# Optimization experiments

Measured on AMD Instinct MI355X. Metric: run time of the kernel, lower is better.

Reference implementation:

```python
import jax, jax.numpy as jnp
import numpy as np

N, E, F_IN, DIM, G = 50000, 800000, 128, 128, 512
NUM_GC_LAYERS = 3
S2S_STEPS = 3


def setup_inputs() -> dict:
    key = jax.random.key(0)
    ks = jax.random.split(key, 17)
    s = 0.05
    rn = lambda k, shape: jax.random.normal(k, shape, jnp.float32) * s
    x = jax.random.normal(ks[0], (N, F_IN), jnp.float32)
    edge_index = jax.random.randint(ks[1], (2, E), 0, N)
    batch = jnp.sort(jax.random.randint(ks[2], (N,), 0, G))
    return dict(
        x=x, edge_index=edge_index, batch=batch,
        lin0_W=rn(ks[3], (DIM, F_IN)), lin0_b=rn(ks[4], (DIM,)),
        gin_W1=rn(ks[5], (DIM, DIM)), gin_b1=rn(ks[6], (DIM,)),
        gin_W2=rn(ks[7], (DIM, DIM)), gin_b2=rn(ks[8], (DIM,)),
        gru_Wih=rn(ks[9], (3 * DIM, DIM)), gru_Whh=rn(ks[10], (3 * DIM, DIM)),
        gru_bih=rn(ks[11], (3 * DIM,)), gru_bhh=rn(ks[12], (3 * DIM,)),
        lstm_Wih=rn(ks[13], (4 * DIM, 2 * DIM)), lstm_Whh=rn(ks[14], (4 * DIM, DIM)),
        lstm_bih=rn(ks[15], (4 * DIM,)), lstm_bhh=rn(ks[16], (4 * DIM,)),
    )


def reference(x, edge_index, batch, lin0_W, lin0_b, gin_W1, gin_b1, gin_W2, gin_b2,
              gru_Wih, gru_Whh, gru_bih, gru_bhh,
              lstm_Wih, lstm_Whh, lstm_bih, lstm_bhh):
    src, dst = edge_index[0], edge_index[1]
    out = jax.nn.relu(x @ lin0_W.T + lin0_b)          # [N, DIM]
    h = out                                            # GRU hidden (seq_len=1, 1 layer)
    for _ in range(NUM_GC_LAYERS):
        # GINConv, eps=0: nn(x + sum_{j in N(i)} x_j); scatter-add over edge list
        aggr = jax.ops.segment_sum(out[src], dst, num_segments=N)
        z = out + aggr
        m = jax.nn.relu(jax.nn.relu(z @ gin_W1.T + gin_b1) @ gin_W2.T + gin_b2)
        # single GRU step (PyTorch gate order: r, z, n)
        gx = m @ gru_Wih.T + gru_bih
        gh = h @ gru_Whh.T + gru_bhh
        gxr, gxz, gxn = jnp.split(gx, 3, axis=-1)
        ghr, ghz, ghn = jnp.split(gh, 3, axis=-1)
        r = jax.nn.sigmoid(gxr + ghr)
        zt = jax.nn.sigmoid(gxz + ghz)
        n = jnp.tanh(gxn + r * ghn)
        h = (1.0 - zt) * n + zt * h
        out = h
    # Set2Set pooling (processing_steps=3), LSTM(2*DIM -> DIM), gate order i,f,g,o
    q_star = jnp.zeros((G, 2 * DIM), x.dtype)
    hl = jnp.zeros((G, DIM), x.dtype)
    cl = jnp.zeros((G, DIM), x.dtype)
    for _ in range(S2S_STEPS):
        gates = q_star @ lstm_Wih.T + lstm_bih + hl @ lstm_Whh.T + lstm_bhh
        i, f, g, o = jnp.split(gates, 4, axis=-1)
        cl = jax.nn.sigmoid(f) * cl + jax.nn.sigmoid(i) * jnp.tanh(g)
        hl = jax.nn.sigmoid(o) * jnp.tanh(cl)
        q = hl                                          # [G, DIM]
        e = jnp.sum(out * q[batch], axis=-1)            # [N] attention logits
        emax = jax.lax.stop_gradient(jax.ops.segment_max(e, batch, num_segments=G))
        emax = jnp.where(jnp.isfinite(emax), emax, 0.0)
        a_num = jnp.exp(e - emax[batch])
        denom = jax.ops.segment_sum(a_num, batch, num_segments=G)
        a = a_num / (denom[batch] + 1e-16)              # per-graph softmax
        rvec = jax.ops.segment_sum(a[:, None] * out, batch, num_segments=G)
        q_star = jnp.concatenate([q, rvec], axis=-1)    # [G, 2*DIM]
    return (q_star, out)
```

## Files before the change

### kernel.cpp

```cpp
#include <hip/hip_runtime.h>
#include <hip/hip_bf16.h>
#include <math.h>

static constexpr int NN  = 50000;
static constexpr int NE  = 800000;
static constexpr int DIM = 128;
static constexpr int NG  = 512;
static constexpr int NBLK = (NN + 255) / 256;

typedef __attribute__((ext_vector_type(8))) short bf16x8;
typedef __attribute__((ext_vector_type(4))) float f32x4;
typedef __attribute__((ext_vector_type(8))) float f32x8;

__device__ __forceinline__ float sigm(float x) {
    return __builtin_amdgcn_rcpf(1.0f + __expf(-x));
}
__device__ __forceinline__ float ftanh(float x) {
    x = fminf(fmaxf(x, -15.f), 15.f);
    float t = __expf(2.f * x);
    return (t - 1.f) * __builtin_amdgcn_rcpf(t + 1.f);
}
__device__ __forceinline__ float b2f(ushort u) { return __uint_as_float(((unsigned)u) << 16); }
__device__ __forceinline__ ushort f2b(float f) {
    __hip_bfloat16 h = __float2bfloat16(f);
    return *reinterpret_cast<ushort*>(&h);
}
__device__ __forceinline__ bf16x8 ldb8(const ushort* p) {
    return *reinterpret_cast<const bf16x8*>(p);
}
__device__ __forceinline__ f32x8 acc8(f32x8 a, uint4 v) {
    a[0] += b2f(v.x & 0xffff); a[1] += b2f(v.x >> 16);
    a[2] += b2f(v.y & 0xffff); a[3] += b2f(v.y >> 16);
    a[4] += b2f(v.z & 0xffff); a[5] += b2f(v.z >> 16);
    a[6] += b2f(v.w & 0xffff); a[7] += b2f(v.w >> 16);
    return a;
}

__global__ __launch_bounds__(256) void k_prep(const float* __restrict__ lin0_W,
                                              const float* __restrict__ gin_W1,
                                              const float* __restrict__ gin_W2,
                                              const float* __restrict__ gru_Wih,
                                              const float* __restrict__ gru_Whh,
                                              const float* __restrict__ gru_bih,
                                              const float* __restrict__ gru_bhh,
                                              const float* __restrict__ lstm_Wih,
                                              const float* __restrict__ lstm_Whh,
                                              const float* __restrict__ lstm_bih,
                                              const float* __restrict__ lstm_bhh,
                                              const int* __restrict__ batch,
                                              ushort* __restrict__ wlin0,
                                              ushort* __restrict__ wg1,
                                              ushort* __restrict__ wg2,
                                              ushort* __restrict__ wihb,
                                              ushort* __restrict__ whhb,
                                              ushort* __restrict__ wrz,
                                              float* __restrict__ brz,
                                              unsigned* __restrict__ wp,
                                              float* __restrict__ bl,
                                              int* __restrict__ gstart,
                                              int* __restrict__ bcnt) {
    const int S0 = 16384, S1 = S0 + 16384, S2 = S1 + 16384;
    const int S3 = S2 + 49152, S4 = S3 + 49152, S5 = S4 + 65536;
    const int S6 = S5 + 256, S7 = S6 + 98304, S8 = S7 + 512;
    const int S9 = S8 + (NG + 1), S10 = S9 + 256;
    int i = blockIdx.x * 256 + threadIdx.x;
    if (i < S0) { wlin0[i] = f2b(lin0_W[i]); }
    else if (i < S1) { int j = i - S0; wg1[j] = f2b(gin_W1[j]); }
    else if (i < S2) { int j = i - S1; wg2[j] = f2b(gin_W2[j]); }
    else if (i < S3) { int j = i - S2; wihb[j] = f2b(gru_Wih[j]); }
    else if (i < S4) { int j = i - S3; whhb[j] = f2b(gru_Whh[j]); }
    else if (i < S5) {
        int j = i - S4; int col = j >> 8, k = j & 255;
        int row = (col >> 7) * 128 + (col & 127);
        wrz[j] = f2b((k < 128) ? gru_Whh[row * 128 + k] : gru_Wih[row * 128 + (k - 128)]);
    }
    else if (i < S6) { int j = i - S5; brz[j] = gru_bih[j] + gru_bhh[j]; }
    else if (i < S7) {
        int j = i - S6; int pk = j / 512, col = j % 512;
        int k0 = 2 * pk, k1 = 2 * pk + 1;
        float v0 = (k0 < 256) ? lstm_Wih[(size_t)col * 256 + k0]
                              : lstm_Whh[(size_t)col * 128 + (k0 - 256)];
        float v1 = (k1 < 256) ? lstm_Wih[(size_t)col * 256 + k1]
                              : lstm_Whh[(size_t)col * 128 + (k1 - 256)];
        wp[j] = ((unsigned)f2b(v1) << 16) | (unsigned)f2b(v0);
    }
    else if (i < S8) { int j = i - S7; bl[j] = lstm_bih[j] + lstm_bhh[j]; }
    else if (i < S9) {
        int g = i - S8;
        int lo = 0, hi = NN;
        while (lo < hi) { int mid = (lo + hi) >> 1; if (batch[mid] < g) lo = mid + 1; else hi = mid; }
        gstart[g] = lo;
    }
    else if (i < S10) { bcnt[i - S9] = 0; }
}
static constexpr int PREP_TOTAL = 16384 * 3 + 49152 * 2 + 65536 + 256 + 98304 + 512 + (NG + 1) + 256;

__global__ __launch_bounds__(256) void k_bcount(const int* __restrict__ dst,
                                                int* __restrict__ bcnt, int e) {
    __shared__ int l[256];
    int tid = threadIdx.x;
    l[tid] = 0;
    __syncthreads();
    int base = blockIdx.x * 4096;
    #pragma unroll
    for (int k = 0; k < 16; ++k) {
        int e0 = base + k * 256 + tid;
        if (e0 < e) atomicAdd(&l[dst[e0] >> 8], 1);
    }
    __syncthreads();
    if (l[tid] > 0) atomicAdd(&bcnt[tid], l[tid]);
}

__global__ __launch_bounds__(256) void k_btop(const int* __restrict__ bcnt,
                                              int* __restrict__ bbase,
                                              int* __restrict__ bcur) {
    __shared__ int s[256];
    int t = threadIdx.x;
    int v = bcnt[t];
    s[t] = v;
    __syncthreads();
    #pragma unroll
    for (int off = 1; off < 256; off <<= 1) {
        int x = (t >= off) ? s[t - off] : 0;
        __syncthreads();
        s[t] += x;
        __syncthreads();
    }
    int ex = s[t] - v;
    bbase[t] = ex;
    bcur[t] = ex;
    if (t == 255) bbase[256] = s[255];
}

__global__ __launch_bounds__(256) void k_bucket_lin0(const int* __restrict__ src,
                                                     const int* __restrict__ dst,
                                                     int* __restrict__ bcur,
                                                     int2* __restrict__ pairs, int e,
                                                     const float* __restrict__ X,
                                                     const ushort* __restrict__ W,
                                                     const float* __restrict__ bias,
                                                     ushort* __restrict__ AB, int n) {
    if (blockIdx.x < (unsigned)NBLK) {
        __shared__ int lcnt[256];
        __shared__ int lbase[256];
        int tid = threadIdx.x;
        lcnt[tid] = 0;
        __syncthreads();
        int base = blockIdx.x * 4096;
        #pragma unroll
        for (int k = 0; k < 16; ++k) {
            int e0 = base + k * 256 + tid;
            if (e0 < e) atomicAdd(&lcnt[dst[e0] >> 8], 1);
        }
        __syncthreads();
        int cnt = lcnt[tid];
        if (cnt > 0) lbase[tid] = atomicAdd(&bcur[tid], cnt);
        __syncthreads();
        lcnt[tid] = 0;
        __syncthreads();
        #pragma unroll
        for (int k = 0; k < 16; ++k) {
            int e0 = base + k * 256 + tid;
            if (e0 < e) {
                int d = dst[e0];
                int b = d >> 8;
                int off = atomicAdd(&lcnt[b], 1);
                pairs[lbase[b] + off] = make_int2(src[e0], d);
            }
        }
        return;
    }
    int bid = blockIdx.x - NBLK;
    int nlb = gridDim.x - NBLK;
    int lane = threadIdx.x & 63, wave = threadIdx.x >> 6;
    int c0 = lane & 15, kg = (lane >> 4) * 8;
    int tb0 = wave * 32;
    bf16x8 B[2][4];
    #pragma unroll
    for (int t = 0; t < 2; ++t)
        #pragma unroll
        for (int kk = 0; kk < 4; ++kk)
            B[t][kk] = ldb8(W + (size_t)(tb0 + t * 16 + c0) * 128 + kk * 32 + kg);

    for (int m0 = bid * 64; m0 < n; m0 += nlb * 64) {
        f32x4 acc[4][2];
        #pragma unroll
        for (int m = 0; m < 4; ++m) { acc[m][0] = {0,0,0,0}; acc[m][1] = {0,0,0,0}; }
        #pragma unroll
        for (int kk = 0; kk < 4; ++kk) {
            #pragma unroll
            for (int m = 0; m < 4; ++m) {
                int ar = min(m0 + m * 16 + c0, n - 1);
                const float* a = X + (size_t)ar * 128 + kk * 32 + kg;
                float4 x0 = *reinterpret_cast<const float4*>(a);
                float4 x1 = *reinterpret_cast<const float4*>(a + 4);
                bf16x8 af;
                af[0] = (short)f2b(x0.x); af[1] = (short)f2b(x0.y);
                af[2] = (short)f2b(x0.z); af[3] = (short)f2b(x0.w);
                af[4] = (short)f2b(x1.x); af[5] = (short)f2b(x1.y);
                af[6] = (short)f2b(x1.z); af[7] = (short)f2b(x1.w);
                acc[m][0] = __builtin_amdgcn_mfma_f32_16x16x32_bf16(af, B[0][kk], acc[m][0], 0, 0, 0);
                acc[m][1] = __builtin_amdgcn_mfma_f32_16x16x32_bf16(af, B[1][kk], acc[m][1], 0, 0, 0);
            }
        }
        #pragma unroll
        for (int m = 0; m < 4; ++m) {
            int rbase = m0 + m * 16 + ((lane >> 4) << 2);
            #pragma unroll
            for (int t = 0; t < 2; ++t) {
                int col = tb0 + t * 16 + c0;
                float bv = bias[col];
                #pragma unroll
                for (int j = 0; j < 4; ++j) {
                    int row = rbase + j;
                    if (row < n) {
                        float v = fmaxf(acc[m][t][j] + bv, 0.f);
                        AB[(size_t)row * 128 + col] = f2b(v);
                    }
                }
            }
        }
    }
}

__global__ __launch_bounds__(256) void k_fillbkt2(const int2* __restrict__ pairs,
                                                  const int* __restrict__ bbase,
                                                  int* __restrict__ rowptr,
                                                  int* __restrict__ csr) {
    __shared__ int lcnt[256];
    __shared__ int s[256];
    __shared__ int lcur[256];
    int b = blockIdx.x, tid = threadIdx.x;
    int w0 = b << 8;
    int r0 = bbase[b], r1 = bbase[b + 1];
    lcnt[tid] = 0;
    __syncthreads();
    for (int i = r0 + tid; i < r1; i += 256)
        atomicAdd(&lcnt[pairs[i].y - w0], 1);
    __syncthreads();
    int v = lcnt[tid];
    s[tid] = v;
    __syncthreads();
    #pragma unroll
    for (int off = 1; off < 256; off <<= 1) {
        int x = (tid >= off) ? s[tid - off] : 0;
        __syncthreads();
        s[tid] += x;
        __syncthreads();
    }
    int ex = r0 + s[tid] - v;
    lcur[tid] = ex;
    if (w0 + tid < NN) rowptr[w0 + tid] = ex;
    if (b == 0 && tid == 0) rowptr[NN] = NE;
    __syncthreads();
    for (int i = r0 + tid; i < r1; i += 256) {
        int2 p = pairs[i];
        int pos = atomicAdd(&lcur[p.y - w0], 1);
        csr[pos] = p.x;
    }
}

__global__ __launch_bounds__(512) void k_aggmlp(const ushort* __restrict__ AB,
                                                const int* __restrict__ rowptr,
                                                const int* __restrict__ csr,
                                                const ushort* __restrict__ W1,
                                                const float* __restrict__ b1,
                                                const ushort* __restrict__ W2,
                                                const float* __restrict__ b2,
                                                ushort* __restrict__ mt, int n) {
    __shared__ ushort Z_lds[32 * 136];
    __shared__ ushort M_lds[32 * 136];
    int tid = threadIdx.x;
    int lane = tid & 63, wave = tid >> 6;
    int c0 = lane & 15, kg = (lane >> 4) * 8;
    int colw = wave * 16 + c0;
    int rj = (lane >> 4) << 2;
    int grow_r = tid >> 4;
    int segi = tid & 15;
    const int stride = gridDim.x * 32;

    bf16x8 B1[4], B2[4];
    #pragma unroll
    for (int kk = 0; kk < 4; ++kk) {
        B1[kk] = ldb8(W1 + (size_t)colw * 128 + kk * 32 + kg);
        B2[kk] = ldb8(W2 + (size_t)colw * 128 + kk * 32 + kg);
    }
    float bv1 = b1[colw], bv2 = b2[colw];
    const uint4* bp = (const uint4*)AB;

    for (int m0 = blockIdx.x * 32; m0 < n; m0 += stride) {
        f32x8 A0 = {0,0,0,0,0,0,0,0};
        int grow = m0 + grow_r;
        if (grow < n) {
            f32x8 A1 = {0,0,0,0,0,0,0,0}, A2 = {0,0,0,0,0,0,0,0}, A3 = {0,0,0,0,0,0,0,0};
            A0 = acc8(A0, bp[(size_t)grow * 16 + segi]);
            int p = rowptr[grow], p1 = rowptr[grow + 1];
            for (; p + 4 <= p1; p += 4) {
                uint4 v0 = bp[(size_t)csr[p + 0] * 16 + segi];
                uint4 v1 = bp[(size_t)csr[p + 1] * 16 + segi];
                uint4 v2 = bp[(size_t)csr[p + 2] * 16 + segi];
                uint4 v3 = bp[(size_t)csr[p + 3] * 16 + segi];
                A0 = acc8(A0, v0); A1 = acc8(A1, v1);
                A2 = acc8(A2, v2); A3 = acc8(A3, v3);
            }
            for (; p < p1; ++p) A0 = acc8(A0, bp[(size_t)csr[p] * 16 + segi]);
            #pragma unroll
            for (int i = 0; i < 8; ++i) A0[i] += A1[i] + A2[i] + A3[i];
        }
        bf16x8 zz;
        #pragma unroll
        for (int i = 0; i < 8; ++i) zz[i] = (short)f2b(A0[i]);
        *reinterpret_cast<bf16x8*>(&Z_lds[grow_r * 136 + segi * 8]) = zz;
        __syncthreads();
        {
            f32x4 a[2] = {{0,0,0,0},{0,0,0,0}};
            #pragma unroll
            for (int kk = 0; kk < 4; ++kk) {
                bf16x8 f0 = *reinterpret_cast<const bf16x8*>(&Z_lds[c0 * 136 + kk * 32 + kg]);
                bf16x8 f1 = *reinterpret_cast<const bf16x8*>(&Z_lds[(16 + c0) * 136 + kk * 32 + kg]);
                a[0] = __builtin_amdgcn_mfma_f32_16x16x32_bf16(f0, B1[kk], a[0], 0, 0, 0);
                a[1] = __builtin_amdgcn_mfma_f32_16x16x32_bf16(f1, B1[kk], a[1], 0, 0, 0);
            }
            #pragma unroll
            for (int m = 0; m < 2; ++m)
                #pragma unroll
                for (int j = 0; j < 4; ++j)
                    M_lds[(m * 16 + rj + j) * 136 + colw] = f2b(fmaxf(a[m][j] + bv1, 0.f));
        }
        __syncthreads();
        {
            f32x4 a[2] = {{0,0,0,0},{0,0,0,0}};
            #pragma unroll
            for (int kk = 0; kk < 4; ++kk) {
                bf16x8 f0 = *reinterpret_cast<const bf16x8*>(&M_lds[c0 * 136 + kk * 32 + kg]);
                bf16x8 f1 = *reinterpret_cast<const bf16x8*>(&M_lds[(16 + c0) * 136 + kk * 32 + kg]);
                a[0] = __builtin_amdgcn_mfma_f32_16x16x32_bf16(f0, B2[kk], a[0], 0, 0, 0);
                a[1] = __builtin_amdgcn_mfma_f32_16x16x32_bf16(f1, B2[kk], a[1], 0, 0, 0);
            }
            #pragma unroll
            for (int m = 0; m < 2; ++m)
                #pragma unroll
                for (int j = 0; j < 4; ++j) {
                    int gr2 = m0 + m * 16 + rj + j;
                    if (gr2 < n)
                        mt[(size_t)gr2 * 128 + colw] = f2b(fmaxf(a[m][j] + bv2, 0.f));
                }
        }
        __syncthreads();
    }
}

template<bool WRITEH>
__global__ __launch_bounds__(512) void k_gru3b(const ushort* __restrict__ ABin,
                                               const ushort* __restrict__ mt,
                                               const ushort* __restrict__ wrz,
                                               const float* __restrict__ brz,
                                               const ushort* __restrict__ Wn,
                                               const ushort* __restrict__ Un,
                                               const float* __restrict__ bin,
                                               const float* __restrict__ bhn,
                                               float* __restrict__ Hf,
                                               ushort* __restrict__ ABout, int n) {
    __shared__ ushort A_lds[32 * 264];
    int tid = threadIdx.x;
    int lane = tid & 63, wave = tid >> 6;
    int c0 = lane & 15, kg = (lane >> 4) * 8;
    int colw = wave * 16 + c0;
    int rj = (lane >> 4) << 2;
    int srow = tid >> 4, scol = (tid & 15) * 8;
    const int stride = gridDim.x * 32;

    bf16x8 Brz[2][8];
    #pragma unroll
    for (int kk = 0; kk < 8; ++kk) {
        Brz[0][kk] = ldb8(wrz + (size_t)(colw) * 256 + kk * 32 + kg);
        Brz[1][kk] = ldb8(wrz + (size_t)(128 + colw) * 256 + kk * 32 + kg);
    }
    bf16x8 Bn[4], Bu[4];
    #pragma unroll
    for (int kk = 0; kk < 4; ++kk) {
        Bn[kk] = ldb8(Wn + (size_t)colw * 128 + kk * 32 + kg);
        Bu[kk] = ldb8(Un + (size_t)colw * 128 + kk * 32 + kg);
    }
    float biN = bin[colw], bhN = bhn[colw];
    float brzR = brz[colw], brzZ = brz[128 + colw];

    int m0 = blockIdx.x * 32;
    bf16x8 ph, pm;
    if (m0 < n) {
        int gr = min(m0 + srow, n - 1);
        ph = ldb8(ABin + (size_t)gr * 128 + scol);
        pm = ldb8(mt + (size_t)gr * 128 + scol);
    }
    for (; m0 < n; m0 += stride) {
        *reinterpret_cast<bf16x8*>(&A_lds[srow * 264 + scol]) = ph;
        *reinterpret_cast<bf16x8*>(&A_lds[srow * 264 + 128 + scol]) = pm;
        __syncthreads();
        int mn = m0 + stride;
        if (mn < n) {
            int gr = min(mn + srow, n - 1);
            ph = ldb8(ABin + (size_t)gr * 128 + scol);
            pm = ldb8(mt + (size_t)gr * 128 + scol);
        }
        f32x4 aR[2] = {{0,0,0,0},{0,0,0,0}};
        f32x4 aZ[2] = {{0,0,0,0},{0,0,0,0}};
        #pragma unroll
        for (int kk = 0; kk < 8; ++kk) {
            bf16x8 f0 = *reinterpret_cast<const bf16x8*>(&A_lds[c0 * 264 + kk * 32 + kg]);
            bf16x8 f1 = *reinterpret_cast<const bf16x8*>(&A_lds[(16 + c0) * 264 + kk * 32 + kg]);
            aR[0] = __builtin_amdgcn_mfma_f32_16x16x32_bf16(f0, Brz[0][kk], aR[0], 0, 0, 0);
            aZ[0] = __builtin_amdgcn_mfma_f32_16x16x32_bf16(f0, Brz[1][kk], aZ[0], 0, 0, 0);
            aR[1] = __builtin_amdgcn_mfma_f32_16x16x32_bf16(f1, Brz[0][kk], aR[1], 0, 0, 0);
            aZ[1] = __builtin_amdgcn_mfma_f32_16x16x32_bf16(f1, Brz[1][kk], aZ[1], 0, 0, 0);
        }
        f32x4 an[2] = {{0,0,0,0},{0,0,0,0}};
        f32x4 au[2] = {{0,0,0,0},{0,0,0,0}};
        #pragma unroll
        for (int kk = 0; kk < 4; ++kk) {
            bf16x8 am0 = *reinterpret_cast<const bf16x8*>(&A_lds[c0 * 264 + 128 + kk * 32 + kg]);
            bf16x8 ah0 = *reinterpret_cast<const bf16x8*>(&A_lds[c0 * 264 + kk * 32 + kg]);
            bf16x8 am1 = *reinterpret_cast<const bf16x8*>(&A_lds[(16 + c0) * 264 + 128 + kk * 32 + kg]);
            bf16x8 ah1 = *reinterpret_cast<const bf16x8*>(&A_lds[(16 + c0) * 264 + kk * 32 + kg]);
            an[0] = __builtin_amdgcn_mfma_f32_16x16x32_bf16(am0, Bn[kk], an[0], 0, 0, 0);
            au[0] = __builtin_amdgcn_mfma_f32_16x16x32_bf16(ah0, Bu[kk], au[0], 0, 0, 0);
            an[1] = __builtin_amdgcn_mfma_f32_16x16x32_bf16(am1, Bn[kk], an[1], 0, 0, 0);
            au[1] = __builtin_amdgcn_mfma_f32_16x16x32_bf16(ah1, Bu[kk], au[1], 0, 0, 0);
        }
        #pragma unroll
        for (int m = 0; m < 2; ++m)
            #pragma unroll
            for (int j = 0; j < 4; ++j) {
                int row = m * 16 + rj + j;
                int grow = m0 + row;
                if (grow < n) {
                    float r  = sigm(aR[m][j] + brzR);
                    float zt = sigm(aZ[m][j] + brzZ);
                    float hold = b2f(A_lds[row * 264 + colw]);
                    float nn = ftanh(an[m][j] + biN + r * (au[m][j] + bhN));
                    float hn = (1.f - zt) * nn + zt * hold;
                    ABout[(size_t)grow * 128 + colw] = f2b(hn);
                    if (WRITEH) Hf[(size_t)grow * 128 + colw] = hn;
                }
            }
        __syncthreads();
    }
}

__global__ __launch_bounds__(512) void k_s2s3(const ushort* __restrict__ AB,
                                              const unsigned* __restrict__ Wp,
                                              const float* __restrict__ bl,
                                              const int* __restrict__ gstart,
                                              float* __restrict__ qout) {
    int g = blockIdx.x, tid = threadIdx.x, lane = tid & 63, wave = tid >> 6;
    __shared__ float qh[384];
    __shared__ float cl_s[128];
    __shared__ float gbuf[512];
    __shared__ float q[128];
    __shared__ float wm[8];
    __shared__ float sw[8];
    __shared__ float rv[8][128];
    if (tid < 384) qh[tid] = 0.f;
    if (tid < 128) cl_s[tid] = 0.f;
    int s = gstart[g], e = gstart[g + 1];

    for (int st = 0; st < 3; ++st) {
        __syncthreads();
        float acc = bl[tid];
        #pragma unroll 8
        for (int pk = 0; pk < 192; ++pk) {
            unsigned u = Wp[pk * 512 + tid];
            acc += b2f(u & 0xffff) * qh[2 * pk] + b2f(u >> 16) * qh[2 * pk + 1];
        }
        gbuf[tid] = acc;
        __syncthreads();
        if (tid < 128) {
            float iv = sigm(gbuf[tid]);
            float fv = sigm(gbuf[128 + tid]);
            float gv = ftanh(gbuf[256 + tid]);
            float ov = sigm(gbuf[384 + tid]);
            float cn = fv * cl_s[tid] + iv * gv;
            cl_s[tid] = cn;
            float hn = ov * ftanh(cn);
            q[tid] = hn;
            qh[256 + tid] = hn;
        }
        __syncthreads();
        float q0 = q[2 * lane], q1 = q[2 * lane + 1];
        float mx = -1e30f, sumw = 0.f, a0 = 0.f, a1 = 0.f;
        for (int node = s + wave; node < e; node += 8) {
            unsigned u = ((const unsigned*)AB)[(size_t)node * 64 + lane];
            float v0 = b2f(u & 0xffff), v1 = b2f(u >> 16);
            float p = v0 * q0 + v1 * q1;
            #pragma unroll
            for (int off = 1; off < 64; off <<= 1) p += __shfl_xor(p, off);
            float nm = fmaxf(mx, p);
            float corr = __expf(mx - nm);
            float wgt = __expf(p - nm);
            sumw = sumw * corr + wgt;
            a0 = a0 * corr + wgt * v0;
            a1 = a1 * corr + wgt * v1;
            mx = nm;
        }
        if (lane == 0) wm[wave] = mx;
        __syncthreads();
        float gm = fmaxf(fmaxf(fmaxf(wm[0], wm[1]), fmaxf(wm[2], wm[3])),
                         fmaxf(fmaxf(wm[4], wm[5]), fmaxf(wm[6], wm[7])));
        float cw = __expf(mx - gm);
        rv[wave][2 * lane] = a0 * cw;
        rv[wave][2 * lane + 1] = a1 * cw;
        if (lane == 0) sw[wave] = sumw * cw;
        __syncthreads();
        if (tid < 128) {
            float r = 0.f, d = 1e-16f;
            #pragma unroll
            for (int wv = 0; wv < 8; ++wv) r += rv[wv][tid];
            #pragma unroll
            for (int wv = 0; wv < 8; ++wv) d += sw[wv];
            if (st == 2) {
                qout[(size_t)g * 256 + tid] = q[tid];
                qout[(size_t)g * 256 + 128 + tid] = r / d;
            } else {
                qh[tid] = q[tid];
                qh[128 + tid] = r / d;
            }
        }
    }
}

extern "C" void kernel_launch(void* const* d_in, const int* in_sizes, int n_in,
                              void* d_out, int out_size, void* d_ws, size_t ws_size,
                              hipStream_t stream) {
    const float* x        = (const float*)d_in[0];
    const int*   ei       = (const int*)d_in[1];
    const int*   batch    = (const int*)d_in[2];
    const float* lin0_W   = (const float*)d_in[3];
    const float* lin0_b   = (const float*)d_in[4];
    const float* gin_W1   = (const float*)d_in[5];
    const float* gin_b1   = (const float*)d_in[6];
    const float* gin_W2   = (const float*)d_in[7];
    const float* gin_b2   = (const float*)d_in[8];
    const float* gru_Wih  = (const float*)d_in[9];
    const float* gru_Whh  = (const float*)d_in[10];
    const float* gru_bih  = (const float*)d_in[11];
    const float* gru_bhh  = (const float*)d_in[12];
    const float* lstm_Wih = (const float*)d_in[13];
    const float* lstm_Whh = (const float*)d_in[14];
    const float* lstm_bih = (const float*)d_in[15];
    const float* lstm_bhh = (const float*)d_in[16];

    float* qstar_out = (float*)d_out;
    float* h         = (float*)d_out + (size_t)NG * 2 * DIM;

    char* w = (char*)d_ws;
    ushort* AB0   = (ushort*)w; w += (size_t)NN * 128 * 2;
    ushort* AB1   = (ushort*)w; w += (size_t)NN * 128 * 2;
    ushort* mt    = (ushort*)w; w += (size_t)NN * 128 * 2;
    ushort* wlin0 = (ushort*)w; w += 16384 * 2;
    ushort* wg1   = (ushort*)w; w += 16384 * 2;
    ushort* wg2   = (ushort*)w; w += 16384 * 2;
    ushort* wihb  = (ushort*)w; w += 49152 * 2;
    ushort* whhb  = (ushort*)w; w += 49152 * 2;
    ushort* wrz   = (ushort*)w; w += 65536 * 2;
    float* brz    = (float*)w;  w += 256 * 4;
    unsigned* wp  = (unsigned*)w; w += (size_t)98304 * 4;
    float* bl     = (float*)w;  w += 512 * 4;
    int* rowptr   = (int*)w;    w += (size_t)(NN + 1) * 4;
    int* bcnt     = (int*)w;    w += 256 * 4;
    int* bbase    = (int*)w;    w += 257 * 4;
    int* bcur     = (int*)w;    w += 256 * 4;
    int* csr_src  = (int*)w;    w += (size_t)NE * 4;
    int2* pairs   = (int2*)w;   w += (size_t)NE * 8;
    int* gstart   = (int*)w;    w += (size_t)(NG + 1) * 4;

    const int* src = ei;
    const int* dst = ei + NE;

    k_prep<<<(PREP_TOTAL + 255) / 256, 256, 0, stream>>>(
        lin0_W, gin_W1, gin_W2, gru_Wih, gru_Whh, gru_bih, gru_bhh,
        lstm_Wih, lstm_Whh, lstm_bih, lstm_bhh, batch,
        wlin0, wg1, wg2, wihb, whhb, wrz, brz, wp, bl, gstart, bcnt);

    k_bcount<<<(NE + 4095) / 4096, 256, 0, stream>>>(dst, bcnt, NE);
    k_btop<<<1, 256, 0, stream>>>(bcnt, bbase, bcur);
    k_bucket_lin0<<<NBLK + 782, 256, 0, stream>>>(src, dst, bcur, pairs, NE,
                                                  x, wlin0, lin0_b, AB0, NN);
    k_fillbkt2<<<NBLK, 256, 0, stream>>>(pairs, bbase, rowptr, csr_src);

    for (int t = 0; t < 3; ++t) {
        ushort* ABc = (t & 1) ? AB1 : AB0;
        ushort* ABn = (t & 1) ? AB0 : AB1;
        k_aggmlp<<<1024, 512, 0, stream>>>(ABc, rowptr, csr_src,
                                           wg1, gin_b1, wg2, gin_b2, mt, NN);
        if (t < 2)
            k_gru3b<false><<<512, 512, 0, stream>>>(ABc, mt, wrz, brz,
                                                    wihb + 256 * 128, whhb + 256 * 128,
                                                    gru_bih + 256, gru_bhh + 256, h, ABn, NN);
        else
            k_gru3b<true><<<512, 512, 0, stream>>>(ABc, mt, wrz, brz,
                                                   wihb + 256 * 128, whhb + 256 * 128,
                                                   gru_bih + 256, gru_bhh + 256, h, ABn, NN);
    }
    const ushort* ABfin = AB1;

    k_s2s3<<<NG, 512, 0, stream>>>(ABfin, wp, bl, gstart, qstar_out);
}
```

Baseline: 338.4 us.

## Process two graphs per block in Set2Set kernel to share LSTM weight loads

The Set2Set kernel now handles two graphs per 512-thread block. Each thread computes LSTM gate dot products for both graphs from a single bf16 weight load, using interleaved LDS state read as float4. The attention/readout pass splits the block's 8 waves into two groups of 4, one group per graph. This halves the global weight traffic and the grid size, but each graph's node scan now has half as many waves and only 256 blocks are launched.

Result: slower. 353.4 us (+4.4%).

```diff
diff --git a/kernel.cpp b/kernel.cpp
--- a/kernel.cpp
+++ b/kernel.cpp
@@ -446,48 +446,56 @@
     }
 }
 
-__global__ __launch_bounds__(512) void k_s2s3(const ushort* __restrict__ AB,
-                                              const unsigned* __restrict__ Wp,
-                                              const float* __restrict__ bl,
-                                              const int* __restrict__ gstart,
-                                              float* __restrict__ qout) {
-    int g = blockIdx.x, tid = threadIdx.x, lane = tid & 63, wave = tid >> 6;
-    __shared__ float qh[384];
-    __shared__ float cl_s[128];
-    __shared__ float gbuf[512];
-    __shared__ float q[128];
-    __shared__ float wm[8];
-    __shared__ float sw[8];
-    __shared__ float rv[8][128];
-    if (tid < 384) qh[tid] = 0.f;
-    if (tid < 128) cl_s[tid] = 0.f;
-    int s = gstart[g], e = gstart[g + 1];
+__global__ __launch_bounds__(512) void k_s2s3b(const ushort* __restrict__ AB,
+                                               const unsigned* __restrict__ Wp,
+                                               const float* __restrict__ bl,
+                                               const int* __restrict__ gstart,
+                                               float* __restrict__ qout) {
+    int gb = blockIdx.x * 2;
+    int tid = threadIdx.x, lane = tid & 63, wave = tid >> 6;
+    __shared__ __align__(16) float qh2[384][2];
+    __shared__ float cl2[128][2];
+    __shared__ float gb2[512][2];
+    __shared__ float q2[128][2];
+    __shared__ float wm2[2][4];
+    __shared__ float sw2[2][4];
+    __shared__ float rv2[2][4][128];
+    if (tid < 384) { qh2[tid][0] = 0.f; qh2[tid][1] = 0.f; }
+    if (tid < 128) { cl2[tid][0] = 0.f; cl2[tid][1] = 0.f; }
+    int gg_w = wave >> 2;
+    int wsub = wave & 3;
+    int s = gstart[gb + gg_w], e = gstart[gb + gg_w + 1];
 
     for (int st = 0; st < 3; ++st) {
         __syncthreads();
-        float acc = bl[tid];
+        float acc0 = bl[tid], acc1 = acc0;
         #pragma unroll 8
         for (int pk = 0; pk < 192; ++pk) {
             unsigned u = Wp[pk * 512 + tid];
-            acc += b2f(u & 0xffff) * qh[2 * pk] + b2f(u >> 16) * qh[2 * pk + 1];
-        }
-        gbuf[tid] = acc;
-        __syncthreads();
-        if (tid < 128) {
-            float iv = sigm(gbuf[tid]);
-            float fv = sigm(gbuf[128 + tid]);
-            float gv = ftanh(gbuf[256 + tid]);
-            float ov = sigm(gbuf[384 + tid]);
-            float cn = fv * cl_s[tid] + iv * gv;
-            cl_s[tid] = cn;
+            float w0 = b2f(u & 0xffff), w1 = b2f(u >> 16);
+            float4 qq = *reinterpret_cast<const float4*>(&qh2[2 * pk][0]);
+            acc0 += w0 * qq.x + w1 * qq.z;
+            acc1 += w0 * qq.y + w1 * qq.w;
+        }
+        gb2[tid][0] = acc0;
+        gb2[tid][1] = acc1;
+        __syncthreads();
+        if (tid < 256) {
+            int gg = tid >> 7, col = tid & 127;
+            float iv = sigm(gb2[col][gg]);
+            float fv = sigm(gb2[128 + col][gg]);
+            float gv = ftanh(gb2[256 + col][gg]);
+            float ov = sigm(gb2[384 + col][gg]);
+            float cn = fv * cl2[col][gg] + iv * gv;
+            cl2[col][gg] = cn;
             float hn = ov * ftanh(cn);
-            q[tid] = hn;
-            qh[256 + tid] = hn;
-        }
-        __syncthreads();
-        float q0 = q[2 * lane], q1 = q[2 * lane + 1];
+            q2[col][gg] = hn;
+            qh2[256 + col][gg] = hn;
+        }
+        __syncthreads();
+        float q0 = q2[2 * lane][gg_w], q1 = q2[2 * lane + 1][gg_w];
         float mx = -1e30f, sumw = 0.f, a0 = 0.f, a1 = 0.f;
-        for (int node = s + wave; node < e; node += 8) {
+        for (int node = s + wsub; node < e; node += 4) {
             unsigned u = ((const unsigned*)AB)[(size_t)node * 64 + lane];
             float v0 = b2f(u & 0xffff), v1 = b2f(u >> 16);
             float p = v0 * q0 + v1 * q1;
@@ -501,27 +509,25 @@
             a1 = a1 * corr + wgt * v1;
             mx = nm;
         }
-        if (lane == 0) wm[wave] = mx;
-        __syncthreads();
-        float gm = fmaxf(fmaxf(fmaxf(wm[0], wm[1]), fmaxf(wm[2], wm[3])),
-                         fmaxf(fmaxf(wm[4], wm[5]), fmaxf(wm[6], wm[7])));
+        if (lane == 0) wm2[gg_w][wsub] = mx;
+        __syncthreads();
+        float gm = fmaxf(fmaxf(wm2[gg_w][0], wm2[gg_w][1]),
+                         fmaxf(wm2[gg_w][2], wm2[gg_w][3]));
         float cw = __expf(mx - gm);
-        rv[wave][2 * lane] = a0 * cw;
-        rv[wave][2 * lane + 1] = a1 * cw;
-        if (lane == 0) sw[wave] = sumw * cw;
-        __syncthreads();
-        if (tid < 128) {
-            float r = 0.f, d = 1e-16f;
-            #pragma unroll
-            for (int wv = 0; wv < 8; ++wv) r += rv[wv][tid];
-            #pragma unroll
-            for (int wv = 0; wv < 8; ++wv) d += sw[wv];
+        rv2[gg_w][wsub][2 * lane] = a0 * cw;
+        rv2[gg_w][wsub][2 * lane + 1] = a1 * cw;
+        if (lane == 0) sw2[gg_w][wsub] = sumw * cw;
+        __syncthreads();
+        if (tid < 256) {
+            int gg = tid >> 7, col = tid & 127;
+            float r = rv2[gg][0][col] + rv2[gg][1][col] + rv2[gg][2][col] + rv2[gg][3][col];
+            float d = sw2[gg][0] + sw2[gg][1] + sw2[gg][2] + sw2[gg][3] + 1e-16f;
             if (st == 2) {
-                qout[(size_t)g * 256 + tid] = q[tid];
-                qout[(size_t)g * 256 + 128 + tid] = r / d;
+                qout[(size_t)(gb + gg) * 256 + col] = q2[col][gg];
+                qout[(size_t)(gb + gg) * 256 + 128 + col] = r / d;
             } else {
-                qh[tid] = q[tid];
-                qh[128 + tid] = r / d;
+                qh2[col][gg] = q2[col][gg];
+                qh2[128 + col][gg] = r / d;
             }
         }
     }
@@ -602,5 +608,5 @@
     }
     const ushort* ABfin = AB1;
 
-    k_s2s3<<<NG, 512, 0, stream>>>(ABfin, wp, bl, gstart, qstar_out);
-}
+    k_s2s3b<<<NG / 2, 512, 0, stream>>>(ABfin, wp, bl, gstart, qstar_out);
+}
```
